# Performance work log

Hardware: AMD Instinct MI355X
Metric: run time of the kernel (lower is better)

## Reference

```python
import jax, jax.numpy as jnp
import numpy as np

EPSILON = 0.01  # from init_kwargs

def setup_inputs() -> dict:
    key = jax.random.key(0)
    k1, k2, k3, k4 = jax.random.split(key, 4)
    N, E, D = 100000, 3200000, 4
    x = jax.random.normal(k1, (N, D), dtype=jnp.float32)
    edge_index = jax.random.randint(k2, (2, E), 0, N, dtype=jnp.int32)
    boo_values = jax.random.normal(k3, (E, D, D), dtype=jnp.float32)
    mask = jnp.ones((N, 1), dtype=jnp.float32)
    diag = jax.random.uniform(k4, (N, D), dtype=jnp.float32)
    return {"x": x, "edge_index": edge_index, "boo_values": boo_values,
            "mask": mask, "diag": diag}

def reference(x, edge_index, boo_values, mask, diag):
    # y = eps*diag*x + A @ (diag * (A^T @ x)), A blocked-sparse with
    # per-edge blocks A_{row,col} = boo_values[e] in R^{DxD}.
    N = x.shape[0]
    row, col = edge_index[0], edge_index[1]
    # spmv_t (A^T x): gather x at row i, message A_ij^T x_i, scatter-add to col j
    msg_t = jnp.einsum('eji,ej->ei', boo_values, x[row])  # [E, D]
    AT_x = jax.ops.segment_sum(msg_t, col, num_segments=N) * mask  # [N, D]
    eps_x = EPSILON * x
    AT_x = AT_x * diag
    eps_x = eps_x * diag
    # spmv (A v): gather v at col j, message A_ij v_j, scatter-add to row i
    msg = jnp.einsum('eij,ej->ei', boo_values, AT_x[col])  # [E, D]
    A_AT_x = jax.ops.segment_sum(msg, row, num_segments=N) * mask  # [N, D]
    return eps_x + A_AT_x
```

## Files before the change

kernel.cpp:

```cpp
#include <hip/hip_runtime.h>
#include <hip/hip_bf16.h>

#define EPSILON 0.01f

__global__ void __launch_bounds__(256) spmvt_kernel(
    const float4* __restrict__ boo,
    const int* __restrict__ row,
    const int* __restrict__ col,
    const float* __restrict__ x,
    float* __restrict__ ATx,
    long long E)
{
    long long t = (long long)blockIdx.x * blockDim.x + threadIdx.x;
    long long e = t >> 2;
    int j = (int)(t & 3);
    if (e >= E) return;

    float4 b = boo[e * 4 + j];
    int r = row[e];
    float xj = x[r * 4 + j];

    float4 p;
    p.x = b.x * xj; p.y = b.y * xj; p.z = b.z * xj; p.w = b.w * xj;

    p.x += __shfl_xor(p.x, 1); p.y += __shfl_xor(p.y, 1);
    p.z += __shfl_xor(p.z, 1); p.w += __shfl_xor(p.w, 1);
    p.x += __shfl_xor(p.x, 2); p.y += __shfl_xor(p.y, 2);
    p.z += __shfl_xor(p.z, 2); p.w += __shfl_xor(p.w, 2);

    float v = (j == 0) ? p.x : (j == 1) ? p.y : (j == 2) ? p.z : p.w;
    int c = col[e];
    unsafeAtomicAdd(&ATx[c * 4 + j], v);
}

__global__ void __launch_bounds__(256) scale_init_kernel(
    const float* __restrict__ x,
    const float* __restrict__ mask,
    const float* __restrict__ diag,
    float* __restrict__ ATx,
    float* __restrict__ out,
    int N)
{
    int n = blockIdx.x * blockDim.x + threadIdx.x;
    if (n >= N) return;
    const float4* x4 = (const float4*)x;
    const float4* d4 = (const float4*)diag;
    float4* a4 = (float4*)ATx;
    float4* o4 = (float4*)out;

    float m = mask[n];
    float4 xv = x4[n];
    float4 dv = d4[n];
    float4 av = a4[n];

    float4 ov;
    ov.x = EPSILON * xv.x * dv.x; ov.y = EPSILON * xv.y * dv.y;
    ov.z = EPSILON * xv.z * dv.z; ov.w = EPSILON * xv.w * dv.w;
    o4[n] = ov;

    float4 sv;
    sv.x = av.x * dv.x * m; sv.y = av.y * dv.y * m;
    sv.z = av.z * dv.z * m; sv.w = av.w * dv.w * m;
    a4[n] = sv;
}

__global__ void __launch_bounds__(256) spmv_kernel(
    const float4* __restrict__ boo,
    const int* __restrict__ row,
    const int* __restrict__ col,
    const float* __restrict__ vv,
    const float* __restrict__ mask,
    float* __restrict__ out,
    long long E)
{
    long long t = (long long)blockIdx.x * blockDim.x + threadIdx.x;
    long long e = t >> 2;
    int i = (int)(t & 3);
    if (e >= E) return;

    float4 b = boo[e * 4 + i];
    int c = col[e];
    const float4* v4 = (const float4*)vv;
    float4 v = v4[c];

    float mi = b.x * v.x + b.y * v.y + b.z * v.z + b.w * v.w;
    int r = row[e];
    float mr = mask[r];
    unsafeAtomicAdd(&out[r * 4 + i], mi * mr);
}

extern "C" void kernel_launch(void* const* d_in, const int* in_sizes, int n_in,
                              void* d_out, int out_size, void* d_ws, size_t ws_size,
                              hipStream_t stream) {
    const float* x    = (const float*)d_in[0];
    const int*   ei   = (const int*)d_in[1];
    const float* boo  = (const float*)d_in[2];
    const float* mask = (const float*)d_in[3];
    const float* diag = (const float*)d_in[4];
    float* out = (float*)d_out;

    int N = in_sizes[0] / 4;
    long long E = in_sizes[1] / 2;
    const int* row = ei;
    const int* col = ei + E;
    float* ATx = (float*)d_ws;

    hipMemsetAsync(ATx, 0, (size_t)N * 4 * sizeof(float), stream);

    const int blk = 256;
    long long T = E * 4;
    int gEdge = (int)((T + blk - 1) / blk);
    int gNode = (N + blk - 1) / blk;

    spmvt_kernel<<<gEdge, blk, 0, stream>>>(
        (const float4*)boo, row, col, x, ATx, E);
    scale_init_kernel<<<gNode, blk, 0, stream>>>(
        x, mask, diag, ATx, out, N);
    spmv_kernel<<<gEdge, blk, 0, stream>>>(
        (const float4*)boo, row, col, ATx, mask, out, E);
}
```

Baseline: 544.7 us.

## Use one thread per edge and privatize scatter-add into replicated accumulators

```diff
diff --git a/kernel.cpp b/kernel.cpp
--- a/kernel.cpp
+++ b/kernel.cpp
@@ -1,92 +1,115 @@
 #include <hip/hip_runtime.h>
-#include <hip/hip_bf16.h>
 
 #define EPSILON 0.01f
+
 
 __global__ void __launch_bounds__(256) spmvt_kernel(
     const float4* __restrict__ boo,
     const int* __restrict__ row,
     const int* __restrict__ col,
-    const float* __restrict__ x,
-    float* __restrict__ ATx,
+    const float4* __restrict__ x4,
+    float* __restrict__ atx,
+    long long n4,
+    int nrep,
     long long E)
 {
-    long long t = (long long)blockIdx.x * blockDim.x + threadIdx.x;
-    long long e = t >> 2;
-    int j = (int)(t & 3);
+    long long e = (long long)blockIdx.x * blockDim.x + threadIdx.x;
     if (e >= E) return;
 
-    float4 b = boo[e * 4 + j];
+    const float4* B = boo + e * 4;
+    float4 b0 = B[0], b1 = B[1], b2 = B[2], b3 = B[3];
     int r = row[e];
-    float xj = x[r * 4 + j];
+    int c = col[e];
+    float4 xv = x4[r];
 
-    float4 p;
-    p.x = b.x * xj; p.y = b.y * xj; p.z = b.z * xj; p.w = b.w * xj;
+    float4 m;
+    m.x = b0.x*xv.x + b1.x*xv.y + b2.x*xv.z + b3.x*xv.w;
+    m.y = b0.y*xv.x + b1.y*xv.y + b2.y*xv.z + b3.y*xv.w;
+    m.z = b0.z*xv.x + b1.z*xv.y + b2.z*xv.z + b3.z*xv.w;
+    m.w = b0.w*xv.x + b1.w*xv.y + b2.w*xv.z + b3.w*xv.w;
 
-    p.x += __shfl_xor(p.x, 1); p.y += __shfl_xor(p.y, 1);
-    p.z += __shfl_xor(p.z, 1); p.w += __shfl_xor(p.w, 1);
-    p.x += __shfl_xor(p.x, 2); p.y += __shfl_xor(p.y, 2);
-    p.z += __shfl_xor(p.z, 2); p.w += __shfl_xor(p.w, 2);
-
-    float v = (j == 0) ? p.x : (j == 1) ? p.y : (j == 2) ? p.z : p.w;
-    int c = col[e];
-    unsafeAtomicAdd(&ATx[c * 4 + j], v);
+    float* dst = atx + (long long)(blockIdx.x & (nrep - 1)) * n4 + (long long)c * 4;
+    unsafeAtomicAdd(dst + 0, m.x);
+    unsafeAtomicAdd(dst + 1, m.y);
+    unsafeAtomicAdd(dst + 2, m.z);
+    unsafeAtomicAdd(dst + 3, m.w);
 }
 
-__global__ void __launch_bounds__(256) scale_init_kernel(
-    const float* __restrict__ x,
+__global__ void __launch_bounds__(256) mid_kernel(
+    const float4* __restrict__ x4,
+    const float4* __restrict__ d4,
     const float* __restrict__ mask,
-    const float* __restrict__ diag,
-    float* __restrict__ ATx,
-    float* __restrict__ out,
-    int N)
+    float4* __restrict__ atx,
+    float4* __restrict__ out4,
+    int K, int N)
 {
     int n = blockIdx.x * blockDim.x + threadIdx.x;
     if (n >= N) return;
-    const float4* x4 = (const float4*)x;
-    const float4* d4 = (const float4*)diag;
-    float4* a4 = (float4*)ATx;
-    float4* o4 = (float4*)out;
 
-    float m = mask[n];
+    float4 acc = atx[n];
+    for (int k = 1; k < K; ++k) {
+        float4 t = atx[(size_t)k * N + n];
+        acc.x += t.x; acc.y += t.y; acc.z += t.z; acc.w += t.w;
+    }
+    float mq = mask[n];
+    float4 dv = d4[n];
+    acc.x *= dv.x * mq; acc.y *= dv.y * mq;
+    acc.z *= dv.z * mq; acc.w *= dv.w * mq;
+    atx[n] = acc;
+
     float4 xv = x4[n];
-    float4 dv = d4[n];
-    float4 av = a4[n];
-
-    float4 ov;
-    ov.x = EPSILON * xv.x * dv.x; ov.y = EPSILON * xv.y * dv.y;
-    ov.z = EPSILON * xv.z * dv.z; ov.w = EPSILON * xv.w * dv.w;
-    o4[n] = ov;
-
-    float4 sv;
-    sv.x = av.x * dv.x * m; sv.y = av.y * dv.y * m;
-    sv.z = av.z * dv.z * m; sv.w = av.w * dv.w * m;
-    a4[n] = sv;
+    float4 o;
+    o.x = EPSILON * xv.x * dv.x; o.y = EPSILON * xv.y * dv.y;
+    o.z = EPSILON * xv.z * dv.z; o.w = EPSILON * xv.w * dv.w;
+    out4[n] = o;
 }
 
 __global__ void __launch_bounds__(256) spmv_kernel(
     const float4* __restrict__ boo,
     const int* __restrict__ row,
     const int* __restrict__ col,
-    const float* __restrict__ vv,
+    const float4* __restrict__ v4,
     const float* __restrict__ mask,
-    float* __restrict__ out,
+    float* __restrict__ dst,
+    long long n4,
+    int nrep,
     long long E)
 {
-    long long t = (long long)blockIdx.x * blockDim.x + threadIdx.x;
-    long long e = t >> 2;
-    int i = (int)(t & 3);
+    long long e = (long long)blockIdx.x * blockDim.x + threadIdx.x;
     if (e >= E) return;
 
-    float4 b = boo[e * 4 + i];
+    const float4* B = boo + e * 4;
+    float4 b0 = B[0], b1 = B[1], b2 = B[2], b3 = B[3];
     int c = col[e];
-    const float4* v4 = (const float4*)vv;
     float4 v = v4[c];
-
-    float mi = b.x * v.x + b.y * v.y + b.z * v.z + b.w * v.w;
     int r = row[e];
     float mr = mask[r];
-    unsafeAtomicAdd(&out[r * 4 + i], mi * mr);
+
+    float m0 = (b0.x*v.x + b0.y*v.y + b0.z*v.z + b0.w*v.w) * mr;
+    float m1 = (b1.x*v.x + b1.y*v.y + b1.z*v.z + b1.w*v.w) * mr;
+    float m2 = (b2.x*v.x + b2.y*v.y + b2.z*v.z + b2.w*v.w) * mr;
+    float m3 = (b3.x*v.x + b3.y*v.y + b3.z*v.z + b3.w*v.w) * mr;
+
+    float* d = dst + (long long)(blockIdx.x & (nrep - 1)) * n4 + (long long)r * 4;
+    unsafeAtomicAdd(d + 0, m0);
+    unsafeAtomicAdd(d + 1, m1);
+    unsafeAtomicAdd(d + 2, m2);
+    unsafeAtomicAdd(d + 3, m3);
+}
+
+__global__ void __launch_bounds__(256) fin_kernel(
+    const float4* __restrict__ rep,
+    float4* __restrict__ out4,
+    int K, int N)
+{
+    int n = blockIdx.x * blockDim.x + threadIdx.x;
+    if (n >= N) return;
+    float4 acc = out4[n];
+    for (int k = 0; k < K; ++k) {
+        float4 t = rep[(size_t)k * N + n];
+        acc.x += t.x; acc.y += t.y; acc.z += t.z; acc.w += t.w;
+    }
+    out4[n] = acc;
 }
 
 extern "C" void kernel_launch(void* const* d_in, const int* in_sizes, int n_in,
@@ -103,19 +126,41 @@
     long long E = in_sizes[1] / 2;
     const int* row = ei;
     const int* col = ei + E;
-    float* ATx = (float*)d_ws;
 
-    hipMemsetAsync(ATx, 0, (size_t)N * 4 * sizeof(float), stream);
+    size_t perB = (size_t)N * 4 * sizeof(float);
+    long long n4 = (long long)N * 4;
 
+    int K = 0;
+    for (int k = 8; k >= 1; k >>= 1) {
+        if (ws_size >= (size_t)(2 * k) * perB) { K = k; break; }
+    }
+
+    float* atx = (float*)d_ws;
     const int blk = 256;
-    long long T = E * 4;
-    int gEdge = (int)((T + blk - 1) / blk);
+    int gEdge = (int)((E + blk - 1) / blk);
     int gNode = (N + blk - 1) / blk;
 
-    spmvt_kernel<<<gEdge, blk, 0, stream>>>(
-        (const float4*)boo, row, col, x, ATx, E);
-    scale_init_kernel<<<gNode, blk, 0, stream>>>(
-        x, mask, diag, ATx, out, N);
-    spmv_kernel<<<gEdge, blk, 0, stream>>>(
-        (const float4*)boo, row, col, ATx, mask, out, E);
+    if (K >= 1) {
+        float* orep = atx + (size_t)K * n4;
+        hipMemsetAsync(atx, 0, (size_t)(2 * K) * perB, stream);
+
+        spmvt_kernel<<<gEdge, blk, 0, stream>>>(
+            (const float4*)boo, row, col, (const float4*)x, atx, n4, K, E);
+        mid_kernel<<<gNode, blk, 0, stream>>>(
+            (const float4*)x, (const float4*)diag, mask,
+            (float4*)atx, (float4*)out, K, N);
+        spmv_kernel<<<gEdge, blk, 0, stream>>>(
+            (const float4*)boo, row, col, (const float4*)atx, mask, orep, n4, K, E);
+        fin_kernel<<<gNode, blk, 0, stream>>>(
+            (const float4*)orep, (float4*)out, K, N);
+    } else {
+        hipMemsetAsync(atx, 0, perB, stream);
+        spmvt_kernel<<<gEdge, blk, 0, stream>>>(
+            (const float4*)boo, row, col, (const float4*)x, atx, n4, 1, E);
+        mid_kernel<<<gNode, blk, 0, stream>>>(
+            (const float4*)x, (const float4*)diag, mask,
+            (float4*)atx, (float4*)out, 1, N);
+        spmv_kernel<<<gEdge, blk, 0, stream>>>(
+            (const float4*)boo, row, col, (const float4*)atx, mask, out, n4, 1, E);
+    }
 }
```

Measured after the change: 1.500 ms. +175.4%, slower.

## Replace global scatter atomics with per-slice LDS accumulation and staged partial reduction

Applied to the files above, without the earlier changes.

```diff
diff --git a/kernel.cpp b/kernel.cpp
--- a/kernel.cpp
+++ b/kernel.cpp
@@ -1,92 +1,159 @@
 #include <hip/hip_runtime.h>
-#include <hip/hip_bf16.h>
 
 #define EPSILON 0.01f
 
-__global__ void __launch_bounds__(256) spmvt_kernel(
+#define BLK    256
+#define SLICE  4096
+#define SLOG   12
+#define NPA    21
+
+
+template<int PASS, int STAGED>
+__global__ void __launch_bounds__(BLK) edge_slice_kernel(
     const float4* __restrict__ boo,
-    const int* __restrict__ row,
-    const int* __restrict__ col,
-    const float* __restrict__ x,
-    float* __restrict__ ATx,
-    long long E)
-{
-    long long t = (long long)blockIdx.x * blockDim.x + threadIdx.x;
-    long long e = t >> 2;
-    int j = (int)(t & 3);
-    if (e >= E) return;
-
-    float4 b = boo[e * 4 + j];
-    int r = row[e];
-    float xj = x[r * 4 + j];
-
-    float4 p;
-    p.x = b.x * xj; p.y = b.y * xj; p.z = b.z * xj; p.w = b.w * xj;
-
-    p.x += __shfl_xor(p.x, 1); p.y += __shfl_xor(p.y, 1);
-    p.z += __shfl_xor(p.z, 1); p.w += __shfl_xor(p.w, 1);
-    p.x += __shfl_xor(p.x, 2); p.y += __shfl_xor(p.y, 2);
-    p.z += __shfl_xor(p.z, 2); p.w += __shfl_xor(p.w, 2);
-
-    float v = (j == 0) ? p.x : (j == 1) ? p.y : (j == 2) ? p.z : p.w;
-    int c = col[e];
-    unsafeAtomicAdd(&ATx[c * 4 + j], v);
-}
-
-__global__ void __launch_bounds__(256) scale_init_kernel(
-    const float* __restrict__ x,
-    const float* __restrict__ mask,
-    const float* __restrict__ diag,
-    float* __restrict__ ATx,
-    float* __restrict__ out,
-    int N)
-{
-    int n = blockIdx.x * blockDim.x + threadIdx.x;
+    const int*    __restrict__ row,
+    const int*    __restrict__ col,
+    const float4* __restrict__ src,
+    const float*  __restrict__ mask,
+    float*        __restrict__ dst,
+    int N, long long E, int P)
+{
+    __shared__ float acc[SLICE * 4];
+
+    const int s    = blockIdx.x / P;
+    const int p    = blockIdx.x - s * P;
+    const int base = s << SLOG;
+    const int lim  = min(SLICE, N - base);
+
+    for (int i = threadIdx.x; i < SLICE * 4; i += BLK) acc[i] = 0.0f;
+    __syncthreads();
+
+    long long chunk = (((E + P - 1) / P) + 3) & ~3LL;
+    long long start = (long long)p * chunk;
+    long long end   = start + chunk; if (end > E) end = E;
+
+    const int* __restrict__ key = (PASS == 1) ? col : row;
+
+    auto body = [&](long long e, int kk) {
+        const float4* B = boo + e * 4;
+        float4 b0 = B[0], b1 = B[1], b2 = B[2], b3 = B[3];
+        float* a = acc + (kk - base) * 4;
+        if (PASS == 1) {
+            float4 xv = src[row[e]];
+            atomicAdd(a + 0, b0.x*xv.x + b1.x*xv.y + b2.x*xv.z + b3.x*xv.w);
+            atomicAdd(a + 1, b0.y*xv.x + b1.y*xv.y + b2.y*xv.z + b3.y*xv.w);
+            atomicAdd(a + 2, b0.z*xv.x + b1.z*xv.y + b2.z*xv.z + b3.z*xv.w);
+            atomicAdd(a + 3, b0.w*xv.x + b1.w*xv.y + b2.w*xv.z + b3.w*xv.w);
+        } else {
+            float4 v = src[col[e]];
+            atomicAdd(a + 0, b0.x*v.x + b0.y*v.y + b0.z*v.z + b0.w*v.w);
+            atomicAdd(a + 1, b1.x*v.x + b1.y*v.y + b1.z*v.z + b1.w*v.w);
+            atomicAdd(a + 2, b2.x*v.x + b2.y*v.y + b2.z*v.z + b2.w*v.w);
+            atomicAdd(a + 3, b3.x*v.x + b3.y*v.y + b3.z*v.z + b3.w*v.w);
+        }
+    };
+
+    for (long long t0 = start + (long long)threadIdx.x * 4; t0 < end;
+         t0 += (long long)BLK * 4) {
+        if (t0 + 4 <= end) {
+            int4 k = *reinterpret_cast<const int4*>(key + t0);
+            if ((unsigned)(k.x - base) < (unsigned)lim) body(t0 + 0, k.x);
+            if ((unsigned)(k.y - base) < (unsigned)lim) body(t0 + 1, k.y);
+            if ((unsigned)(k.z - base) < (unsigned)lim) body(t0 + 2, k.z);
+            if ((unsigned)(k.w - base) < (unsigned)lim) body(t0 + 3, k.w);
+        } else {
+            for (long long e = t0; e < end; ++e) {
+                int kk = key[e];
+                if ((unsigned)(kk - base) < (unsigned)lim) body(e, kk);
+            }
+        }
+    }
+    __syncthreads();
+
+    if (STAGED) {
+        float* st = dst + ((long long)s * P + p) * (SLICE * 4);
+        for (int f = threadIdx.x; f < lim * 4; f += BLK) st[f] = acc[f];
+    } else if (PASS == 1) {
+        for (int f = threadIdx.x; f < lim * 4; f += BLK)
+            unsafeAtomicAdd(dst + ((long long)base * 4 + f), acc[f]);
+    } else {
+        for (int f = threadIdx.x; f < lim * 4; f += BLK) {
+            float mv = mask[base + (f >> 2)];
+            unsafeAtomicAdd(dst + ((long long)base * 4 + f), acc[f] * mv);
+        }
+    }
+}
+
+__global__ void __launch_bounds__(BLK) mid_staged_kernel(
+    const float4* __restrict__ stage,
+    const float4* __restrict__ d4,
+    const float*  __restrict__ mask,
+    float4* __restrict__ v4,
+    int N, int P)
+{
+    int n = blockIdx.x * BLK + threadIdx.x;
     if (n >= N) return;
-    const float4* x4 = (const float4*)x;
-    const float4* d4 = (const float4*)diag;
-    float4* a4 = (float4*)ATx;
-    float4* o4 = (float4*)out;
-
-    float m = mask[n];
+    int s = n >> SLOG, local = n & (SLICE - 1);
+    const float4* t = stage + (long long)s * P * SLICE + local;
+    float4 a = make_float4(0.f, 0.f, 0.f, 0.f);
+    for (int p = 0; p < P; ++p) {
+        float4 u = t[(long long)p * SLICE];
+        a.x += u.x; a.y += u.y; a.z += u.z; a.w += u.w;
+    }
+    float4 dv = d4[n];
+    float  m  = mask[n];
+    a.x *= dv.x * m; a.y *= dv.y * m; a.z *= dv.z * m; a.w *= dv.w * m;
+    v4[n] = a;
+}
+
+__global__ void __launch_bounds__(BLK) fin_staged_kernel(
+    const float4* __restrict__ stage,
+    const float4* __restrict__ x4,
+    const float4* __restrict__ d4,
+    const float*  __restrict__ mask,
+    float4* __restrict__ out4,
+    int N, int P)
+{
+    int n = blockIdx.x * BLK + threadIdx.x;
+    if (n >= N) return;
+    int s = n >> SLOG, local = n & (SLICE - 1);
+    const float4* t = stage + (long long)s * P * SLICE + local;
+    float4 a = make_float4(0.f, 0.f, 0.f, 0.f);
+    for (int p = 0; p < P; ++p) {
+        float4 u = t[(long long)p * SLICE];
+        a.x += u.x; a.y += u.y; a.z += u.z; a.w += u.w;
+    }
     float4 xv = x4[n];
     float4 dv = d4[n];
-    float4 av = a4[n];
-
-    float4 ov;
-    ov.x = EPSILON * xv.x * dv.x; ov.y = EPSILON * xv.y * dv.y;
-    ov.z = EPSILON * xv.z * dv.z; ov.w = EPSILON * xv.w * dv.w;
-    o4[n] = ov;
-
-    float4 sv;
-    sv.x = av.x * dv.x * m; sv.y = av.y * dv.y * m;
-    sv.z = av.z * dv.z * m; sv.w = av.w * dv.w * m;
-    a4[n] = sv;
-}
-
-__global__ void __launch_bounds__(256) spmv_kernel(
-    const float4* __restrict__ boo,
-    const int* __restrict__ row,
-    const int* __restrict__ col,
-    const float* __restrict__ vv,
-    const float* __restrict__ mask,
-    float* __restrict__ out,
-    long long E)
-{
-    long long t = (long long)blockIdx.x * blockDim.x + threadIdx.x;
-    long long e = t >> 2;
-    int i = (int)(t & 3);
-    if (e >= E) return;
-
-    float4 b = boo[e * 4 + i];
-    int c = col[e];
-    const float4* v4 = (const float4*)vv;
-    float4 v = v4[c];
-
-    float mi = b.x * v.x + b.y * v.y + b.z * v.z + b.w * v.w;
-    int r = row[e];
-    float mr = mask[r];
-    unsafeAtomicAdd(&out[r * 4 + i], mi * mr);
+    float  m  = mask[n];
+    float4 o;
+    o.x = EPSILON * xv.x * dv.x + a.x * m;
+    o.y = EPSILON * xv.y * dv.y + a.y * m;
+    o.z = EPSILON * xv.z * dv.z + a.z * m;
+    o.w = EPSILON * xv.w * dv.w + a.w * m;
+    out4[n] = o;
+}
+
+__global__ void __launch_bounds__(BLK) mid_atomic_kernel(
+    const float4* __restrict__ x4,
+    const float4* __restrict__ d4,
+    const float*  __restrict__ mask,
+    float4* __restrict__ atx,
+    float4* __restrict__ out4,
+    int N)
+{
+    int n = blockIdx.x * BLK + threadIdx.x;
+    if (n >= N) return;
+    float4 a  = atx[n];
+    float4 dv = d4[n];
+    float  m  = mask[n];
+    a.x *= dv.x * m; a.y *= dv.y * m; a.z *= dv.z * m; a.w *= dv.w * m;
+    atx[n] = a;
+    float4 xv = x4[n];
+    float4 o;
+    o.x = EPSILON * xv.x * dv.x; o.y = EPSILON * xv.y * dv.y;
+    o.z = EPSILON * xv.z * dv.z; o.w = EPSILON * xv.w * dv.w;
+    out4[n] = o;
 }
 
 extern "C" void kernel_launch(void* const* d_in, const int* in_sizes, int n_in,
@@ -103,19 +170,39 @@
     long long E = in_sizes[1] / 2;
     const int* row = ei;
     const int* col = ei + E;
-    float* ATx = (float*)d_ws;
-
-    hipMemsetAsync(ATx, 0, (size_t)N * 4 * sizeof(float), stream);
-
-    const int blk = 256;
-    long long T = E * 4;
-    int gEdge = (int)((T + blk - 1) / blk);
-    int gNode = (N + blk - 1) / blk;
-
-    spmvt_kernel<<<gEdge, blk, 0, stream>>>(
-        (const float4*)boo, row, col, x, ATx, E);
-    scale_init_kernel<<<gNode, blk, 0, stream>>>(
-        x, mask, diag, ATx, out, N);
-    spmv_kernel<<<gEdge, blk, 0, stream>>>(
-        (const float4*)boo, row, col, ATx, mask, out, E);
-}
+
+    int S = (N + SLICE - 1) / SLICE;
+    size_t vbytes = (size_t)N * 4 * sizeof(float);
+    size_t tileb  = (size_t)SLICE * 4 * sizeof(float);
+
+    int P = 0;
+    for (int cand = 16; cand >= 2; cand >>= 1)
+        if (ws_size >= vbytes + (size_t)S * cand * tileb) { P = cand; break; }
+
+    float* v = (float*)d_ws;
+    const int gNode = (N + BLK - 1) / BLK;
+
+    if (P > 0) {
+        float* stage = v + (size_t)N * 4;
+        int gEdge = S * P;
+        edge_slice_kernel<1, 1><<<gEdge, BLK, 0, stream>>>(
+            (const float4*)boo, row, col, (const float4*)x, mask, stage, N, E, P);
+        mid_staged_kernel<<<gNode, BLK, 0, stream>>>(
+            (const float4*)stage, (const float4*)diag, mask, (float4*)v, N, P);
+        edge_slice_kernel<2, 1><<<gEdge, BLK, 0, stream>>>(
+            (const float4*)boo, row, col, (const float4*)v, mask, stage, N, E, P);
+        fin_staged_kernel<<<gNode, BLK, 0, stream>>>(
+            (const float4*)stage, (const float4*)x, (const float4*)diag, mask,
+            (float4*)out, N, P);
+    } else {
+        hipMemsetAsync(v, 0, vbytes, stream);
+        int gEdge = S * NPA;
+        edge_slice_kernel<1, 0><<<gEdge, BLK, 0, stream>>>(
+            (const float4*)boo, row, col, (const float4*)x, mask, v, N, E, NPA);
+        mid_atomic_kernel<<<gNode, BLK, 0, stream>>>(
+            (const float4*)x, (const float4*)diag, mask,
+            (float4*)v, (float4*)out, N);
+        edge_slice_kernel<2, 0><<<gEdge, BLK, 0, stream>>>(
+            (const float4*)boo, row, col, (const float4*)v, mask, out, N, E, NPA);
+    }
+}
```

Result: slower. 1.527 ms (+180.2%).
